# Kernel optimization log

Measured on AMD Instinct MI355X. Metric: run time of the kernel, lower is better.

## Reference

```python
import jax, jax.numpy as jnp
import numpy as np

B, T, C, DK = 4096, 33, 512, 64  # batch, seq (== encoder_block_size), n_embd, d_k


def setup_inputs() -> dict:
    key = jax.random.key(0)
    k1, k2, k3, k4 = jax.random.split(key, 4)
    w_scale = 1.0 / np.sqrt(C).astype(np.float32)
    x = jax.random.normal(k1, (B, T, C), dtype=jnp.float32)
    Wq = jax.random.normal(k2, (DK, C), dtype=jnp.float32) * w_scale
    Wk = jax.random.normal(k3, (DK, C), dtype=jnp.float32) * w_scale
    Wv = jax.random.normal(k4, (DK, C), dtype=jnp.float32) * w_scale
    return {"x": x, "Wq": Wq, "Wk": Wk, "Wv": Wv}


def reference(x, Wq, Wk, Wv):
    # nn.Linear(n_embd, d_k, bias=False): y = x @ W.T
    q = jnp.einsum('btc,dc->btd', x, Wq)  # [B,T,DK]
    k = jnp.einsum('btc,dc->btd', x, Wk)
    v = jnp.einsum('btc,dc->btd', x, Wv)
    # NOTE: original scales by C**-0.5 (n_embd), not d_k**-0.5 — keep faithful.
    wei = jnp.einsum('btd,bsd->bts', q, k) * (C ** -0.5)  # [B,T,T]
    tril = jnp.tril(jnp.ones((T, T), dtype=bool))
    wei = jnp.where(tril, wei, -jnp.inf)
    wei = jax.nn.softmax(wei, axis=-1)
    # dropout p=0.0 -> identity
    out = jnp.einsum('bts,bsd->btd', wei, v)  # [B,T,DK]
    return out
```

## Files before the change

kernel.cpp:

```cpp
#include <hip/hip_runtime.h>
#include <hip/hip_bf16.h>


typedef __attribute__((ext_vector_type(8))) short bf16x8;
typedef __attribute__((ext_vector_type(4))) float floatx4;

#define NB 4096
#define TT 33
#define CC 512

#define XS   520
#define QS   72
#define SSTR 36

#define OFF_Q   0
#define OFF_K   4752
#define OFF_VT  9504
#define OFF_P   18720
#define OFF_S   23472
#define SMEM_BYTES 34320

__device__ __forceinline__ ushort f2b(float f) {
    union { __hip_bfloat16 h; ushort u; } cv;
    cv.h = __float2bfloat16(f);
    return cv.u;
}
__device__ __forceinline__ int imin(int a, int b) { return a < b ? a : b; }

__device__ __forceinline__ bf16x8 load8_b(const ushort* p) { return *(const bf16x8*)p; }
__device__ __forceinline__ bf16x8 load8_f(const float* p) {
    float4 f0 = *(const float4*)p;
    float4 f1 = *(const float4*)(p + 4);
    bf16x8 r;
    r[0] = (short)f2b(f0.x); r[1] = (short)f2b(f0.y);
    r[2] = (short)f2b(f0.z); r[3] = (short)f2b(f0.w);
    r[4] = (short)f2b(f1.x); r[5] = (short)f2b(f1.y);
    r[6] = (short)f2b(f1.z); r[7] = (short)f2b(f1.w);
    return r;
}

__global__ void conv_w_kernel(const float* __restrict__ Wq,
                              const float* __restrict__ Wk,
                              const float* __restrict__ Wv,
                              ushort* __restrict__ wb) {
    const float* src = (blockIdx.y == 0) ? Wq : (blockIdx.y == 1) ? Wk : Wv;
    int i = (blockIdx.x * 256 + threadIdx.x) * 4;
    float4 f = *(const float4*)&src[i];
    ushort4 u;
    u.x = f2b(f.x); u.y = f2b(f.y); u.z = f2b(f.z); u.w = f2b(f.w);
    *(ushort4*)&wb[(size_t)blockIdx.y * 32768 + i] = u;
}

template <bool USE_WS>
__global__ __launch_bounds__(256, 4) void head_kernel(
    const float* __restrict__ x,
    const ushort* __restrict__ wb,
    const float* __restrict__ Wqf,
    const float* __restrict__ Wkf,
    const float* __restrict__ Wvf,
    float* __restrict__ out)
{
    __shared__ __align__(16) char smem[SMEM_BYTES];
    ushort* x_s  = (ushort*)smem;
    ushort* q_s  = (ushort*)(smem + OFF_Q);
    ushort* k_s  = (ushort*)(smem + OFF_K);
    ushort* vT_s = (ushort*)(smem + OFF_VT);
    ushort* p_s  = (ushort*)(smem + OFF_P);
    float*  S_s  = (float*)(smem + OFF_S);

    const int b    = blockIdx.x;
    const int tid  = threadIdx.x;
    const int lane = tid & 63;
    const int wave = tid >> 6;
    const int l15  = lane & 15;
    const int quad = lane >> 4;

    const float* xg = x + (size_t)b * (TT * CC);
    for (int i = tid; i < TT * 128; i += 256) {
        int r = i >> 7, c = (i & 127) << 2;
        float4 f = *(const float4*)&xg[r * CC + c];
        ushort4 u;
        u.x = f2b(f.x); u.y = f2b(f.y); u.z = f2b(f.z); u.w = f2b(f.w);
        *(ushort4*)&x_s[r * XS + c] = u;
    }
    __syncthreads();

    floatx4 acc[3][3] = {};
    int nidx[3];
    const ushort* wrow_b[3];
    const float*  wrow_f[3];
    #pragma unroll
    for (int nl = 0; nl < 3; nl++) {
        int n = wave * 3 + nl;
        nidx[nl] = n;
        int mat = n >> 2;
        int row = (n & 3) * 16 + l15;
        if (USE_WS) {
            wrow_b[nl] = wb + (size_t)mat * 32768 + (size_t)row * CC;
            wrow_f[nl] = nullptr;
        } else {
            const float* Wf = (mat == 0) ? Wqf : (mat == 1) ? Wkf : Wvf;
            wrow_f[nl] = Wf + (size_t)row * CC;
            wrow_b[nl] = nullptr;
        }
    }
    {
        const int r0 = l15, r1 = 16 + l15, r2 = 32;
        for (int ks = 0; ks < 16; ks++) {
            int c = ks * 32 + quad * 8;
            bf16x8 a0 = *(const bf16x8*)&x_s[r0 * XS + c];
            bf16x8 a1 = *(const bf16x8*)&x_s[r1 * XS + c];
            bf16x8 a2 = *(const bf16x8*)&x_s[r2 * XS + c];
            bf16x8 b0 = USE_WS ? load8_b(&wrow_b[0][c]) : load8_f(&wrow_f[0][c]);
            bf16x8 b1 = USE_WS ? load8_b(&wrow_b[1][c]) : load8_f(&wrow_f[1][c]);
            bf16x8 b2 = USE_WS ? load8_b(&wrow_b[2][c]) : load8_f(&wrow_f[2][c]);
            acc[0][0] = __builtin_amdgcn_mfma_f32_16x16x32_bf16(a0, b0, acc[0][0], 0, 0, 0);
            acc[1][0] = __builtin_amdgcn_mfma_f32_16x16x32_bf16(a1, b0, acc[1][0], 0, 0, 0);
            acc[2][0] = __builtin_amdgcn_mfma_f32_16x16x32_bf16(a2, b0, acc[2][0], 0, 0, 0);
            acc[0][1] = __builtin_amdgcn_mfma_f32_16x16x32_bf16(a0, b1, acc[0][1], 0, 0, 0);
            acc[1][1] = __builtin_amdgcn_mfma_f32_16x16x32_bf16(a1, b1, acc[1][1], 0, 0, 0);
            acc[2][1] = __builtin_amdgcn_mfma_f32_16x16x32_bf16(a2, b1, acc[2][1], 0, 0, 0);
            acc[0][2] = __builtin_amdgcn_mfma_f32_16x16x32_bf16(a0, b2, acc[0][2], 0, 0, 0);
            acc[1][2] = __builtin_amdgcn_mfma_f32_16x16x32_bf16(a1, b2, acc[1][2], 0, 0, 0);
            acc[2][2] = __builtin_amdgcn_mfma_f32_16x16x32_bf16(a2, b2, acc[2][2], 0, 0, 0);
        }
    }
    __syncthreads();

    for (int i = tid; i < 64 * 32; i += 256) {
        int d = i >> 5, t = i & 31;
        if (t) vT_s[d * QS + 32 + t] = 0;
    }
    #pragma unroll
    for (int nl = 0; nl < 3; nl++) {
        int n = nidx[nl];
        int mat = n >> 2;
        int col = (n & 3) * 16 + l15;
        #pragma unroll
        for (int m = 0; m < 3; m++) {
            #pragma unroll
            for (int r = 0; r < 4; r++) {
                int row = m * 16 + quad * 4 + r;
                if (row < TT) {
                    ushort v = f2b(acc[m][nl][r]);
                    if (mat == 0)      q_s[row * QS + col] = v;
                    else if (mat == 1) k_s[row * QS + col] = v;
                    else               vT_s[col * QS + row] = v;
                }
            }
        }
    }
    __syncthreads();

    const float scale = 0.044194173824159216f;
    for (int g = wave; g < 9; g += 4) {
        int mt = g / 3, nt = g - mt * 3;
        floatx4 s = {};
        int ra = imin(mt * 16 + l15, 32);
        int rb = imin(nt * 16 + l15, 32);
        #pragma unroll
        for (int ks = 0; ks < 2; ks++) {
            int c = ks * 32 + quad * 8;
            bf16x8 aq = *(const bf16x8*)&q_s[ra * QS + c];
            bf16x8 bk = *(const bf16x8*)&k_s[rb * QS + c];
            s = __builtin_amdgcn_mfma_f32_16x16x32_bf16(aq, bk, s, 0, 0, 0);
        }
        #pragma unroll
        for (int r = 0; r < 4; r++) {
            int row = mt * 16 + quad * 4 + r;
            int col = nt * 16 + l15;
            if (row < TT && col < TT) S_s[row * SSTR + col] = s[r] * scale;
        }
    }
    __syncthreads();

    if (tid < TT) {
        const float* Sr = &S_s[tid * SSTR];
        float4 f[9];
        #pragma unroll
        for (int j = 0; j < 9; j++) f[j] = *(const float4*)&Sr[4 * j];
        const float* fv = (const float*)f;
        float mx = -1e30f;
        #pragma unroll
        for (int c = 0; c < TT; c++)
            mx = fmaxf(mx, (c <= tid) ? fv[c] : -1e30f);
        float e[TT];
        float sum = 0.f;
        #pragma unroll
        for (int c = 0; c < TT; c++) {
            float t = __expf(fv[c] - mx);
            e[c] = (c <= tid) ? t : 0.f;
            sum += e[c];
        }
        float inv = 1.f / sum;
        ushort* Pr = &p_s[tid * QS];
        #pragma unroll
        for (int j = 0; j < 16; j++) {
            uint pk = (uint)f2b(e[2 * j] * inv) | ((uint)f2b(e[2 * j + 1] * inv) << 16);
            *(uint*)&Pr[2 * j] = pk;
        }
        Pr[32] = f2b(e[32] * inv);
        Pr[33] = 0;
        #pragma unroll
        for (int j = 0; j < 15; j++)
            *(uint*)&Pr[34 + 2 * j] = 0u;
    }
    __syncthreads();

    float* og = out + (size_t)b * (TT * 64);
    for (int g = wave; g < 12; g += 4) {
        int mt = g >> 2, nt = g & 3;
        floatx4 o = {};
        int ra = imin(mt * 16 + l15, 32);
        int rb = nt * 16 + l15;
        #pragma unroll
        for (int ks = 0; ks < 2; ks++) {
            int c = ks * 32 + quad * 8;
            bf16x8 ap = *(const bf16x8*)&p_s[ra * QS + c];
            bf16x8 bv = *(const bf16x8*)&vT_s[rb * QS + c];
            o = __builtin_amdgcn_mfma_f32_16x16x32_bf16(ap, bv, o, 0, 0, 0);
        }
        #pragma unroll
        for (int r = 0; r < 4; r++) {
            int t = mt * 16 + quad * 4 + r;
            if (t < TT) og[t * 64 + nt * 16 + l15] = o[r];
        }
    }
}

extern "C" void kernel_launch(void* const* d_in, const int* in_sizes, int n_in,
                              void* d_out, int out_size, void* d_ws, size_t ws_size,
                              hipStream_t stream) {
    const float* x  = (const float*)d_in[0];
    const float* Wq = (const float*)d_in[1];
    const float* Wk = (const float*)d_in[2];
    const float* Wv = (const float*)d_in[3];
    float* out = (float*)d_out;

    if (ws_size >= 3u * 64u * 512u * sizeof(ushort)) {
        ushort* wb = (ushort*)d_ws;
        conv_w_kernel<<<dim3(32, 3), 256, 0, stream>>>(Wq, Wk, Wv, wb);
        head_kernel<true><<<NB, 256, 0, stream>>>(x, wb, nullptr, nullptr, nullptr, out);
    } else {
        head_kernel<false><<<NB, 256, 0, stream>>>(x, nullptr, Wq, Wk, Wv, out);
    }
}
```

Measured before the change: 463.3 us.

## Compute attention scores and softmax redundantly per wave in registers

Each wave now computes the full 33x33 QK^T score tile in registers, applies the causal mask and does the softmax with lane shuffles. It then writes bf16 unnormalized probabilities to a per-wave shared buffer and computes its own 16-column slice of P·V, applying the 1/sum normalization at output. This removes two block barriers, the fp32 score round-trip through shared memory, and the single 33-thread softmax stage. In exchange, QK^T MFMA work is duplicated four times and shared memory use grows. The x load is also restructured to issue all global loads before any conversion, to get more memory-level parallelism.

Result: faster. 452.0 us (-2.4%).

```diff
diff --git a/kernel.cpp b/kernel.cpp
--- a/kernel.cpp
+++ b/kernel.cpp
@@ -9,16 +9,13 @@
 #define TT 33
 #define CC 512
 
-#define XS   520
-#define QS   72
-#define SSTR 36
-
-#define OFF_Q   0
-#define OFF_K   4752
-#define OFF_VT  9504
-#define OFF_P   18720
-#define OFF_S   23472
-#define SMEM_BYTES 34320
+#define XS 520
+#define QS 72
+#define OFF_Q  0
+#define OFF_K  4752
+#define OFF_VT 9504
+#define OFF_P  18720
+#define SMEM_BYTES 37728
 
 __device__ __forceinline__ ushort f2b(float f) {
     union { __hip_bfloat16 h; ushort u; } cv;
@@ -65,8 +62,6 @@
     ushort* q_s  = (ushort*)(smem + OFF_Q);
     ushort* k_s  = (ushort*)(smem + OFF_K);
     ushort* vT_s = (ushort*)(smem + OFF_VT);
-    ushort* p_s  = (ushort*)(smem + OFF_P);
-    float*  S_s  = (float*)(smem + OFF_S);
 
     const int b    = blockIdx.x;
     const int tid  = threadIdx.x;
@@ -75,13 +70,27 @@
     const int l15  = lane & 15;
     const int quad = lane >> 4;
 
+    ushort* Pw = (ushort*)(smem + OFF_P) + wave * (TT * QS);
+
     const float* xg = x + (size_t)b * (TT * CC);
-    for (int i = tid; i < TT * 128; i += 256) {
-        int r = i >> 7, c = (i & 127) << 2;
-        float4 f = *(const float4*)&xg[r * CC + c];
-        ushort4 u;
-        u.x = f2b(f.x); u.y = f2b(f.y); u.z = f2b(f.z); u.w = f2b(f.w);
-        *(ushort4*)&x_s[r * XS + c] = u;
+    {
+        float4 buf[17];
+        #pragma unroll
+        for (int j = 0; j < 17; j++) {
+            int i = tid + j * 256;
+            if (i < 4224) buf[j] = ((const float4*)xg)[i];
+        }
+        #pragma unroll
+        for (int j = 0; j < 17; j++) {
+            int i = tid + j * 256;
+            if (i < 4224) {
+                int r = i >> 7, c = (i & 127) << 2;
+                ushort4 u;
+                u.x = f2b(buf[j].x); u.y = f2b(buf[j].y);
+                u.z = f2b(buf[j].z); u.w = f2b(buf[j].w);
+                *(ushort4*)&x_s[r * XS + c] = u;
+            }
+        }
     }
     __syncthreads();
 
@@ -152,78 +161,86 @@
     }
     __syncthreads();
 
+    bf16x8 aq[3][2], bk[3][2];
+    #pragma unroll
+    for (int m = 0; m < 3; m++) {
+        int rr = imin(m * 16 + l15, 32);
+        aq[m][0] = *(const bf16x8*)&q_s[rr * QS + quad * 8];
+        aq[m][1] = *(const bf16x8*)&q_s[rr * QS + 32 + quad * 8];
+        bk[m][0] = *(const bf16x8*)&k_s[rr * QS + quad * 8];
+        bk[m][1] = *(const bf16x8*)&k_s[rr * QS + 32 + quad * 8];
+    }
+    floatx4 s[3][3] = {};
+    #pragma unroll
+    for (int mt = 0; mt < 3; mt++)
+        #pragma unroll
+        for (int nt = 0; nt < 3; nt++) {
+            s[mt][nt] = __builtin_amdgcn_mfma_f32_16x16x32_bf16(aq[mt][0], bk[nt][0], s[mt][nt], 0, 0, 0);
+            s[mt][nt] = __builtin_amdgcn_mfma_f32_16x16x32_bf16(aq[mt][1], bk[nt][1], s[mt][nt], 0, 0, 0);
+        }
+
     const float scale = 0.044194173824159216f;
-    for (int g = wave; g < 9; g += 4) {
-        int mt = g / 3, nt = g - mt * 3;
-        floatx4 s = {};
+    #pragma unroll
+    for (int mt = 0; mt < 3; mt++)
+        #pragma unroll
+        for (int nt = 0; nt < 3; nt++)
+            #pragma unroll
+            for (int r = 0; r < 4; r++) {
+                int row = mt * 16 + quad * 4 + r;
+                int col = nt * 16 + l15;
+                float v = s[mt][nt][r] * scale;
+                s[mt][nt][r] = (col <= row) ? v : -1e30f;
+            }
+    float inv_s[3][4];
+    #pragma unroll
+    for (int mt = 0; mt < 3; mt++)
+        #pragma unroll
+        for (int r = 0; r < 4; r++) {
+            float m = fmaxf(fmaxf(s[mt][0][r], s[mt][1][r]), s[mt][2][r]);
+            #pragma unroll
+            for (int d = 1; d < 16; d <<= 1) m = fmaxf(m, __shfl_xor(m, d));
+            float sum = 0.f;
+            #pragma unroll
+            for (int nt = 0; nt < 3; nt++) {
+                float e = __expf(s[mt][nt][r] - m);
+                s[mt][nt][r] = e;
+                sum += e;
+            }
+            #pragma unroll
+            for (int d = 1; d < 16; d <<= 1) sum += __shfl_xor(sum, d);
+            inv_s[mt][r] = 1.f / sum;
+        }
+
+    for (int i = lane; i < TT * 8; i += 64) {
+        int r = i >> 3, c = 48 + ((i & 7) << 1);
+        *(uint*)&Pw[r * QS + c] = 0u;
+    }
+    #pragma unroll
+    for (int mt = 0; mt < 3; mt++)
+        #pragma unroll
+        for (int nt = 0; nt < 3; nt++)
+            #pragma unroll
+            for (int r = 0; r < 4; r++) {
+                int row = mt * 16 + quad * 4 + r;
+                if (row < TT) Pw[row * QS + nt * 16 + l15] = f2b(s[mt][nt][r]);
+            }
+
+    const int dcol = wave * 16 + l15;
+    bf16x8 bv0 = *(const bf16x8*)&vT_s[dcol * QS + quad * 8];
+    bf16x8 bv1 = *(const bf16x8*)&vT_s[dcol * QS + 32 + quad * 8];
+    float* og = out + (size_t)b * (TT * 64);
+    #pragma unroll
+    for (int mt = 0; mt < 3; mt++) {
         int ra = imin(mt * 16 + l15, 32);
-        int rb = imin(nt * 16 + l15, 32);
-        #pragma unroll
-        for (int ks = 0; ks < 2; ks++) {
-            int c = ks * 32 + quad * 8;
-            bf16x8 aq = *(const bf16x8*)&q_s[ra * QS + c];
-            bf16x8 bk = *(const bf16x8*)&k_s[rb * QS + c];
-            s = __builtin_amdgcn_mfma_f32_16x16x32_bf16(aq, bk, s, 0, 0, 0);
-        }
+        bf16x8 ap0 = *(const bf16x8*)&Pw[ra * QS + quad * 8];
+        bf16x8 ap1 = *(const bf16x8*)&Pw[ra * QS + 32 + quad * 8];
+        floatx4 o = {};
+        o = __builtin_amdgcn_mfma_f32_16x16x32_bf16(ap0, bv0, o, 0, 0, 0);
+        o = __builtin_amdgcn_mfma_f32_16x16x32_bf16(ap1, bv1, o, 0, 0, 0);
         #pragma unroll
         for (int r = 0; r < 4; r++) {
             int row = mt * 16 + quad * 4 + r;
-            int col = nt * 16 + l15;
-            if (row < TT && col < TT) S_s[row * SSTR + col] = s[r] * scale;
-        }
-    }
-    __syncthreads();
-
-    if (tid < TT) {
-        const float* Sr = &S_s[tid * SSTR];
-        float4 f[9];
-        #pragma unroll
-        for (int j = 0; j < 9; j++) f[j] = *(const float4*)&Sr[4 * j];
-        const float* fv = (const float*)f;
-        float mx = -1e30f;
-        #pragma unroll
-        for (int c = 0; c < TT; c++)
-            mx = fmaxf(mx, (c <= tid) ? fv[c] : -1e30f);
-        float e[TT];
-        float sum = 0.f;
-        #pragma unroll
-        for (int c = 0; c < TT; c++) {
-            float t = __expf(fv[c] - mx);
-            e[c] = (c <= tid) ? t : 0.f;
-            sum += e[c];
-        }
-        float inv = 1.f / sum;
-        ushort* Pr = &p_s[tid * QS];
-        #pragma unroll
-        for (int j = 0; j < 16; j++) {
-            uint pk = (uint)f2b(e[2 * j] * inv) | ((uint)f2b(e[2 * j + 1] * inv) << 16);
-            *(uint*)&Pr[2 * j] = pk;
-        }
-        Pr[32] = f2b(e[32] * inv);
-        Pr[33] = 0;
-        #pragma unroll
-        for (int j = 0; j < 15; j++)
-            *(uint*)&Pr[34 + 2 * j] = 0u;
-    }
-    __syncthreads();
-
-    float* og = out + (size_t)b * (TT * 64);
-    for (int g = wave; g < 12; g += 4) {
-        int mt = g >> 2, nt = g & 3;
-        floatx4 o = {};
-        int ra = imin(mt * 16 + l15, 32);
-        int rb = nt * 16 + l15;
-        #pragma unroll
-        for (int ks = 0; ks < 2; ks++) {
-            int c = ks * 32 + quad * 8;
-            bf16x8 ap = *(const bf16x8*)&p_s[ra * QS + c];
-            bf16x8 bv = *(const bf16x8*)&vT_s[rb * QS + c];
-            o = __builtin_amdgcn_mfma_f32_16x16x32_bf16(ap, bv, o, 0, 0, 0);
-        }
-        #pragma unroll
-        for (int r = 0; r < 4; r++) {
-            int t = mt * 16 + quad * 4 + r;
-            if (t < TT) og[t * 64 + nt * 16 + l15] = o[r];
+            if (row < TT) og[row * 64 + dcol] = o[r] * inv_s[mt][r];
         }
     }
 }
```
